# Performance work log

Hardware: AMD Instinct MI355X
Metric: run time of the kernel (lower is better)

Reference implementation:

```python
import jax, jax.numpy as jnp
import numpy as np

NUM_HEADS = 8
DIM_HEAD = 32


def setup_inputs() -> dict:
    key = jax.random.key(0)
    k1, k2, k3 = jax.random.split(key, 3)
    dim = 256
    inner = NUM_HEADS * DIM_HEAD  # 256
    x = jax.random.normal(k1, (2, dim, 32, 32, 32), dtype=jnp.float32)
    # Conv1d(kernel_size=1, bias=False) weights == plain matrices [out_ch, in_ch]
    w_qkv = jax.random.normal(k2, (inner * 3, dim), dtype=jnp.float32) * 0.02
    w_out = jax.random.normal(k3, (dim, inner), dtype=jnp.float32) * 0.02
    return {"x": x, "w_qkv": w_qkv, "w_out": w_out}


def reference(x, w_qkv, w_out):
    b, c, h, w, d = x.shape
    n = h * w * d
    x_flat = x.reshape(b, c, n)
    # 1x1 conv == channel matmul: [b, 3*inner, n]
    qkv = jnp.einsum('oc,bcn->bon', w_qkv, x_flat)
    q, k, v = jnp.split(qkv, 3, axis=1)

    def to_heads(t):  # [b, inner, n] -> [b, H, n, Dh]
        return t.reshape(b, NUM_HEADS, DIM_HEAD, n).transpose(0, 1, 3, 2)

    q = jax.nn.softmax(to_heads(q), axis=-1)   # softmax over dim_head
    k = jax.nn.softmax(to_heads(k), axis=-2)   # softmax over tokens n
    v = to_heads(v)
    # context: [b, H, Dh, Dh]
    context = jnp.einsum('bhnd,bhne->bhde', k, v)
    attn_out = jnp.einsum('bhnd,bhde->bhne', q, context)  # [b, H, n, Dh]
    attn_out = attn_out.transpose(0, 1, 3, 2).reshape(b, NUM_HEADS * DIM_HEAD, n)
    out = jnp.einsum('oi,bin->bon', w_out, attn_out)  # to_out 1x1 conv (dropout=0)
    return out.reshape(b, c, h, w, d)
```

## Files before the change

kernel.cpp:

```cpp
#include <hip/hip_runtime.h>

#define NTOK 32768

typedef __attribute__((ext_vector_type(8))) short  bf16x8;
typedef __attribute__((ext_vector_type(8))) unsigned short u16x8;
typedef __attribute__((ext_vector_type(4))) float  f32x4;

__device__ __forceinline__ unsigned short f32_to_bf16(float f) {
    unsigned int u = __float_as_uint(f);
    u += 0x7FFFu + ((u >> 16) & 1u);
    return (unsigned short)(u >> 16);
}
__device__ __forceinline__ float bf16_to_f32(unsigned short h) {
    return __uint_as_float(((unsigned int)h) << 16);
}

template <typename BT, typename CT, int MCHUNKS, bool QSOFT>
__global__ __launch_bounds__(256) void gemm_bstat(
    const unsigned short* __restrict__ A, const BT* __restrict__ B,
    CT* __restrict__ C, long sA, long sB, long sC)
{
    const int bz = blockIdx.y;
    A += (long)bz * sA; B += (long)bz * sB; C += (long)bz * sC;
    const int col0 = blockIdx.x * 64;

    __shared__ unsigned short Bs[64 * 256];

    const int t = threadIdx.x;
    const int wave = t >> 6, lane = t & 63;
    const int wm = wave >> 1, wn = wave & 1;
    const int m16 = lane & 15, quad = lane >> 4;

    {
        const int n = t & 63;
        const int kg0 = (t >> 6) * 8;
        const int key = n & 7;
        const BT* bcol = B + col0 + n;
        #pragma unroll
        for (int g = 0; g < 8; ++g) {
            const int kg = kg0 + g;
            unsigned short tmp[8];
            #pragma unroll
            for (int i = 0; i < 8; ++i) {
                BT v = bcol[(size_t)(kg * 8 + i) * NTOK];
                if constexpr (sizeof(BT) == 4) tmp[i] = f32_to_bf16((float)v);
                else                           tmp[i] = (unsigned short)v;
            }
            *(u16x8*)&Bs[n * 256 + ((kg ^ key) * 8)] = *(const u16x8*)tmp;
        }
    }
    __syncthreads();

    const int swk = m16 & 7;

    for (int mc = 0; mc < MCHUNKS; ++mc) {
        const int m0 = mc * 128;
        f32x4 acc[4][2] = {};

        const unsigned short* Abase = A + (size_t)(m0 + wm * 64 + m16) * 256 + quad * 8;

        #pragma unroll
        for (int kk = 0; kk < 8; ++kk) {
            bf16x8 bf[2];
            #pragma unroll
            for (int nt = 0; nt < 2; ++nt) {
                const int col = wn * 32 + nt * 16 + m16;
                bf[nt] = *(const bf16x8*)&Bs[col * 256 + (((kk * 4 + quad) ^ swk) * 8)];
            }
            #pragma unroll
            for (int mt = 0; mt < 4; ++mt) {
                const bf16x8 af = *(const bf16x8*)&Abase[(size_t)mt * 16 * 256 + kk * 32];
                #pragma unroll
                for (int nt = 0; nt < 2; ++nt)
                    acc[mt][nt] = __builtin_amdgcn_mfma_f32_16x16x32_bf16(
                        bf[nt], af, acc[mt][nt], 0, 0, 0);
            }
        }

        if (QSOFT && m0 < 256) {
            #pragma unroll
            for (int hj = 0; hj < 2; ++hj) {
                #pragma unroll
                for (int nt = 0; nt < 2; ++nt) {
                    #pragma unroll
                    for (int r = 0; r < 4; ++r) {
                        float mx = fmaxf(acc[hj * 2][nt][r], acc[hj * 2 + 1][nt][r]);
                        mx = fmaxf(mx, __shfl_xor(mx, 1, 64));
                        mx = fmaxf(mx, __shfl_xor(mx, 2, 64));
                        mx = fmaxf(mx, __shfl_xor(mx, 4, 64));
                        mx = fmaxf(mx, __shfl_xor(mx, 8, 64));
                        const float e0 = __expf(acc[hj * 2][nt][r] - mx);
                        const float e1 = __expf(acc[hj * 2 + 1][nt][r] - mx);
                        float s = e0 + e1;
                        s += __shfl_xor(s, 1, 64);
                        s += __shfl_xor(s, 2, 64);
                        s += __shfl_xor(s, 4, 64);
                        s += __shfl_xor(s, 8, 64);
                        const float inv = 1.0f / s;
                        acc[hj * 2][nt][r]     = e0 * inv;
                        acc[hj * 2 + 1][nt][r] = e1 * inv;
                    }
                }
            }
        }

        #pragma unroll
        for (int mt = 0; mt < 4; ++mt) {
            const int row = m0 + wm * 64 + mt * 16 + m16;
            #pragma unroll
            for (int nt = 0; nt < 2; ++nt) {
                const int col = col0 + wn * 32 + nt * 16 + quad * 4;
                if constexpr (sizeof(CT) == 4) {
                    *(float4*)&C[(size_t)row * NTOK + col] =
                        *(const float4*)&acc[mt][nt];
                } else {
                    ushort4 o;
                    o.x = f32_to_bf16(acc[mt][nt][0]);
                    o.y = f32_to_bf16(acc[mt][nt][1]);
                    o.z = f32_to_bf16(acc[mt][nt][2]);
                    o.w = f32_to_bf16(acc[mt][nt][3]);
                    *(ushort4*)&C[(size_t)row * NTOK + col] = o;
                }
            }
        }
    }
}

__global__ __launch_bounds__(256) void cast_bf16_kernel(
    const float* __restrict__ src, unsigned short* __restrict__ dst, int n4)
{
    const int i = blockIdx.x * 256 + threadIdx.x;
    if (i < n4) {
        float4 v = ((const float4*)src)[i];
        ushort4 o;
        o.x = f32_to_bf16(v.x); o.y = f32_to_bf16(v.y);
        o.z = f32_to_bf16(v.z); o.w = f32_to_bf16(v.w);
        ((ushort4*)dst)[i] = o;
    }
}

#define CCHUNK 256
__global__ __launch_bounds__(512) void ctx_mfma_kernel(
    const unsigned short* __restrict__ qkv,
    float* __restrict__ num, float* __restrict__ den)
{
    const int b = blockIdx.y;
    const int n0 = blockIdx.x * CCHUNK;
    const int h = threadIdx.x >> 6;
    const int lane = threadIdx.x & 63;
    const int m16 = lane & 15, quad = lane >> 4;

    const unsigned short* kb =
        qkv + ((long)b * 768 + 256 + h * 32 + m16) * (long)NTOK + n0 + quad * 8;
    const unsigned short* vb =
        qkv + ((long)b * 768 + 512 + h * 32 + m16) * (long)NTOK + n0 + quad * 8;

    f32x4 acc[2][2] = {};
    float dp[2] = {0.f, 0.f};

    #pragma unroll
    for (int n = 0; n < CCHUNK; n += 32) {
        bf16x8 af[2], bfv[2];
        #pragma unroll
        for (int dt = 0; dt < 2; ++dt) {
            const u16x8 kr = *(const u16x8*)(kb + (size_t)dt * 16 * NTOK + n);
            unsigned short tmp[8];
            #pragma unroll
            for (int i = 0; i < 8; ++i) {
                const float e = __expf(bf16_to_f32(kr[i]));
                const unsigned short eb = f32_to_bf16(e);
                tmp[i] = eb;
                dp[dt] += bf16_to_f32(eb);
            }
            af[dt] = *(const bf16x8*)tmp;
        }
        #pragma unroll
        for (int et = 0; et < 2; ++et)
            bfv[et] = *(const bf16x8*)(vb + (size_t)et * 16 * NTOK + n);
        #pragma unroll
        for (int dt = 0; dt < 2; ++dt)
            #pragma unroll
            for (int et = 0; et < 2; ++et)
                acc[dt][et] = __builtin_amdgcn_mfma_f32_16x16x32_bf16(
                    af[dt], bfv[et], acc[dt][et], 0, 0, 0);
    }

    float* nbase = num + ((long)(b * 8 + h) * 32) * 32;
    #pragma unroll
    for (int dt = 0; dt < 2; ++dt)
        #pragma unroll
        for (int et = 0; et < 2; ++et)
            #pragma unroll
            for (int r = 0; r < 4; ++r)
                atomicAdd(&nbase[(dt * 16 + quad * 4 + r) * 32 + et * 16 + m16],
                          acc[dt][et][r]);

    #pragma unroll
    for (int dt = 0; dt < 2; ++dt) {
        float s = dp[dt];
        s += __shfl_xor(s, 16, 64);
        s += __shfl_xor(s, 32, 64);
        if (quad == 0)
            atomicAdd(&den[b * 256 + h * 32 + dt * 16 + m16], s);
    }
}

__global__ __launch_bounds__(256) void combine_kernel(
    const float* __restrict__ w_out, const float* __restrict__ num,
    const float* __restrict__ den, unsigned short* __restrict__ W2)
{
    const int tid = blockIdx.x * 256 + threadIdx.x;
    const int b = tid >> 16;
    const int rem = tid & 65535;
    const int o = rem >> 8;
    const int i = rem & 255;
    const int h = i >> 5, d = i & 31;
    const float* wrow = w_out + o * 256 + h * 32;
    const float* nrow = num + (((long)(b * 8 + h) * 32 + d) << 5);
    float s = 0.f;
    #pragma unroll
    for (int e = 0; e < 32; ++e) s += wrow[e] * nrow[e];
    W2[tid] = f32_to_bf16(s / den[b * 256 + h * 32 + d]);
}

extern "C" void kernel_launch(void* const* d_in, const int* in_sizes, int n_in,
                              void* d_out, int out_size, void* d_ws, size_t ws_size,
                              hipStream_t stream)
{
    const float* x     = (const float*)d_in[0];
    const float* w_qkv = (const float*)d_in[1];
    const float* w_out = (const float*)d_in[2];
    float* out = (float*)d_out;

    unsigned short* qkv_bf = (unsigned short*)d_ws;
    const long qkv_elems = 2L * 768 * NTOK;
    unsigned short* wqkv_bf = qkv_bf + qkv_elems;
    unsigned short* W2 = wqkv_bf + 768 * 256;
    float* num  = (float*)(W2 + 2 * 256 * 256);
    float* den  = num + 16384;

    hipMemsetAsync(num, 0, (16384 + 512) * sizeof(float), stream);

    cast_bf16_kernel<<<192, 256, 0, stream>>>(w_qkv, wqkv_bf, 768 * 256 / 4);

    gemm_bstat<float, unsigned short, 6, true><<<dim3(512, 2), 256, 0, stream>>>(
        wqkv_bf, x, qkv_bf, 0L, 256L * NTOK, 768L * NTOK);

    ctx_mfma_kernel<<<dim3(NTOK / CCHUNK, 2), 512, 0, stream>>>(qkv_bf, num, den);

    combine_kernel<<<512, 256, 0, stream>>>(w_out, num, den, W2);

    gemm_bstat<unsigned short, float, 2, false><<<dim3(512, 2), 256, 0, stream>>>(
        W2, qkv_bf, out, 65536L, 768L * NTOK, 256L * NTOK);
}
```

Measured before the change: 287.4 us.

## Fuse QKV projection with context accumulation, keep K/V in LDS

The QKV GEMM and the K·V context reduction are merged into one kernel. K (after exp) and V tiles stay in shared memory and feed per-strip MFMA context products, so K/V are never written to or re-read from global memory. Q is stored in a strip-major layout so the output GEMM reads its strip contiguously. A-fragment loads are also software-prefetched one k-step ahead. The costs are more LDS per block (about 96KB, which lowers occupancy), many more atomicAdds on num/den (one set per 64-token strip instead of per 256), and extra register pressure.

```diff
diff --git a/kernel.cpp b/kernel.cpp
--- a/kernel.cpp
+++ b/kernel.cpp
@@ -1,6 +1,8 @@
 #include <hip/hip_runtime.h>
 
 #define NTOK 32768
+#define SSTRIP 64
+#define QSTRIDE (256 * SSTRIP)
 
 typedef __attribute__((ext_vector_type(8))) short  bf16x8;
 typedef __attribute__((ext_vector_type(8))) unsigned short u16x8;
@@ -15,16 +17,21 @@
     return __uint_as_float(((unsigned int)h) << 16);
 }
 
-template <typename BT, typename CT, int MCHUNKS, bool QSOFT>
-__global__ __launch_bounds__(256) void gemm_bstat(
-    const unsigned short* __restrict__ A, const BT* __restrict__ B,
-    CT* __restrict__ C, long sA, long sB, long sC)
+__global__ __launch_bounds__(256) void qkv_ctx_kernel(
+    const unsigned short* __restrict__ A,
+    const float* __restrict__ X,
+    unsigned short* __restrict__ Q,
+    float* __restrict__ num, float* __restrict__ den)
 {
     const int bz = blockIdx.y;
-    A += (long)bz * sA; B += (long)bz * sB; C += (long)bz * sC;
-    const int col0 = blockIdx.x * 64;
-
-    __shared__ unsigned short Bs[64 * 256];
+    X += (long)bz * 256 * NTOK;
+    Q += (long)bz * 256 * NTOK;
+    const int strip = blockIdx.x;
+    const int col0 = strip * SSTRIP;
+
+    __shared__ unsigned short Bs[SSTRIP * 256];
+    __shared__ unsigned short Ks[256 * SSTRIP];
+    __shared__ unsigned short Vs[256 * SSTRIP];
 
     const int t = threadIdx.x;
     const int wave = t >> 6, lane = t & 63;
@@ -35,17 +42,14 @@
         const int n = t & 63;
         const int kg0 = (t >> 6) * 8;
         const int key = n & 7;
-        const BT* bcol = B + col0 + n;
+        const float* bcol = X + col0 + n;
         #pragma unroll
         for (int g = 0; g < 8; ++g) {
             const int kg = kg0 + g;
             unsigned short tmp[8];
             #pragma unroll
-            for (int i = 0; i < 8; ++i) {
-                BT v = bcol[(size_t)(kg * 8 + i) * NTOK];
-                if constexpr (sizeof(BT) == 4) tmp[i] = f32_to_bf16((float)v);
-                else                           tmp[i] = (unsigned short)v;
-            }
+            for (int i = 0; i < 8; ++i)
+                tmp[i] = f32_to_bf16(bcol[(size_t)(kg * 8 + i) * NTOK]);
             *(u16x8*)&Bs[n * 256 + ((kg ^ key) * 8)] = *(const u16x8*)tmp;
         }
     }
@@ -53,14 +57,25 @@
 
     const int swk = m16 & 7;
 
-    for (int mc = 0; mc < MCHUNKS; ++mc) {
+    for (int mc = 0; mc < 6; ++mc) {
         const int m0 = mc * 128;
         f32x4 acc[4][2] = {};
 
         const unsigned short* Abase = A + (size_t)(m0 + wm * 64 + m16) * 256 + quad * 8;
 
+        bf16x8 af_cur[4], af_nxt[4];
+        #pragma unroll
+        for (int mt = 0; mt < 4; ++mt)
+            af_cur[mt] = *(const bf16x8*)&Abase[(size_t)mt * 16 * 256];
+
         #pragma unroll
         for (int kk = 0; kk < 8; ++kk) {
+            if (kk < 7) {
+                #pragma unroll
+                for (int mt = 0; mt < 4; ++mt)
+                    af_nxt[mt] = *(const bf16x8*)
+                        &Abase[(size_t)mt * 16 * 256 + (kk + 1) * 32];
+            }
             bf16x8 bf[2];
             #pragma unroll
             for (int nt = 0; nt < 2; ++nt) {
@@ -68,16 +83,16 @@
                 bf[nt] = *(const bf16x8*)&Bs[col * 256 + (((kk * 4 + quad) ^ swk) * 8)];
             }
             #pragma unroll
-            for (int mt = 0; mt < 4; ++mt) {
-                const bf16x8 af = *(const bf16x8*)&Abase[(size_t)mt * 16 * 256 + kk * 32];
+            for (int mt = 0; mt < 4; ++mt)
                 #pragma unroll
                 for (int nt = 0; nt < 2; ++nt)
                     acc[mt][nt] = __builtin_amdgcn_mfma_f32_16x16x32_bf16(
-                        bf[nt], af, acc[mt][nt], 0, 0, 0);
-            }
-        }
-
-        if (QSOFT && m0 < 256) {
+                        bf[nt], af_cur[mt], acc[mt][nt], 0, 0, 0);
+            #pragma unroll
+            for (int mt = 0; mt < 4; ++mt) af_cur[mt] = af_nxt[mt];
+        }
+
+        if (mc < 2) {
             #pragma unroll
             for (int hj = 0; hj < 2; ++hj) {
                 #pragma unroll
@@ -102,25 +117,177 @@
                     }
                 }
             }
-        }
-
-        #pragma unroll
-        for (int mt = 0; mt < 4; ++mt) {
-            const int row = m0 + wm * 64 + mt * 16 + m16;
-            #pragma unroll
-            for (int nt = 0; nt < 2; ++nt) {
-                const int col = col0 + wn * 32 + nt * 16 + quad * 4;
-                if constexpr (sizeof(CT) == 4) {
-                    *(float4*)&C[(size_t)row * NTOK + col] =
-                        *(const float4*)&acc[mt][nt];
-                } else {
+            unsigned short* Qb = Q + (size_t)strip * QSTRIDE;
+            #pragma unroll
+            for (int mt = 0; mt < 4; ++mt) {
+                const int row = m0 + wm * 64 + mt * 16 + m16;
+                #pragma unroll
+                for (int nt = 0; nt < 2; ++nt) {
+                    const int col = wn * 32 + nt * 16 + quad * 4;
                     ushort4 o;
                     o.x = f32_to_bf16(acc[mt][nt][0]);
                     o.y = f32_to_bf16(acc[mt][nt][1]);
                     o.z = f32_to_bf16(acc[mt][nt][2]);
                     o.w = f32_to_bf16(acc[mt][nt][3]);
-                    *(ushort4*)&C[(size_t)row * NTOK + col] = o;
+                    *(ushort4*)&Qb[(size_t)row * SSTRIP + col] = o;
                 }
+            }
+        } else if (mc < 4) {
+            #pragma unroll
+            for (int mt = 0; mt < 4; ++mt) {
+                const int kchan = (m0 - 256) + wm * 64 + mt * 16 + m16;
+                float dp = 0.f;
+                #pragma unroll
+                for (int nt = 0; nt < 2; ++nt) {
+                    ushort4 o;
+                    unsigned short eb;
+                    #pragma unroll
+                    for (int r = 0; r < 4; ++r) {
+                        eb = f32_to_bf16(__expf(acc[mt][nt][r]));
+                        dp += bf16_to_f32(eb);
+                        ((unsigned short*)&o)[r] = eb;
+                    }
+                    const int col = wn * 32 + nt * 16 + quad * 4;
+                    *(ushort4*)&Ks[(size_t)kchan * SSTRIP + col] = o;
+                }
+                dp += __shfl_xor(dp, 16, 64);
+                dp += __shfl_xor(dp, 32, 64);
+                if (quad == 0)
+                    atomicAdd(&den[bz * 256 + kchan], dp);
+            }
+        } else {
+            #pragma unroll
+            for (int mt = 0; mt < 4; ++mt) {
+                const int vchan = (m0 - 512) + wm * 64 + mt * 16 + m16;
+                #pragma unroll
+                for (int nt = 0; nt < 2; ++nt) {
+                    ushort4 o;
+                    o.x = f32_to_bf16(acc[mt][nt][0]);
+                    o.y = f32_to_bf16(acc[mt][nt][1]);
+                    o.z = f32_to_bf16(acc[mt][nt][2]);
+                    o.w = f32_to_bf16(acc[mt][nt][3]);
+                    const int col = wn * 32 + nt * 16 + quad * 4;
+                    *(ushort4*)&Vs[(size_t)vchan * SSTRIP + col] = o;
+                }
+            }
+        }
+    }
+
+    __syncthreads();
+
+    #pragma unroll
+    for (int hh = 0; hh < 2; ++hh) {
+        const int h = wave * 2 + hh;
+        f32x4 cacc[2][2] = {};
+        #pragma unroll
+        for (int ks = 0; ks < 2; ++ks) {
+            bf16x8 kf[2], vf[2];
+            #pragma unroll
+            for (int dt = 0; dt < 2; ++dt)
+                kf[dt] = *(const bf16x8*)
+                    &Ks[(size_t)(h * 32 + dt * 16 + m16) * SSTRIP + ks * 32 + quad * 8];
+            #pragma unroll
+            for (int et = 0; et < 2; ++et)
+                vf[et] = *(const bf16x8*)
+                    &Vs[(size_t)(h * 32 + et * 16 + m16) * SSTRIP + ks * 32 + quad * 8];
+            #pragma unroll
+            for (int dt = 0; dt < 2; ++dt)
+                #pragma unroll
+                for (int et = 0; et < 2; ++et)
+                    cacc[dt][et] = __builtin_amdgcn_mfma_f32_16x16x32_bf16(
+                        kf[dt], vf[et], cacc[dt][et], 0, 0, 0);
+        }
+        float* nbase = num + ((long)(bz * 8 + h) * 32) * 32;
+        #pragma unroll
+        for (int dt = 0; dt < 2; ++dt)
+            #pragma unroll
+            for (int et = 0; et < 2; ++et)
+                #pragma unroll
+                for (int r = 0; r < 4; ++r)
+                    atomicAdd(&nbase[(dt * 16 + quad * 4 + r) * 32 + et * 16 + m16],
+                              cacc[dt][et][r]);
+    }
+}
+
+__global__ __launch_bounds__(256) void gemm_out(
+    const unsigned short* __restrict__ A,
+    const unsigned short* __restrict__ Q,
+    float* __restrict__ C)
+{
+    const int bz = blockIdx.y;
+    A += (long)bz * 65536;
+    Q += (long)bz * 256 * NTOK;
+    C += (long)bz * 256 * NTOK;
+    const int strip = blockIdx.x;
+    const int col0 = strip * SSTRIP;
+
+    __shared__ unsigned short Bs[SSTRIP * 256];
+
+    const int t = threadIdx.x;
+    const int wave = t >> 6, lane = t & 63;
+    const int wm = wave >> 1, wn = wave & 1;
+    const int m16 = lane & 15, quad = lane >> 4;
+
+    {
+        const int n = t & 63;
+        const int kg0 = (t >> 6) * 8;
+        const int key = n & 7;
+        const unsigned short* bcol = Q + (size_t)strip * QSTRIDE + n;
+        #pragma unroll
+        for (int g = 0; g < 8; ++g) {
+            const int kg = kg0 + g;
+            unsigned short tmp[8];
+            #pragma unroll
+            for (int i = 0; i < 8; ++i)
+                tmp[i] = bcol[(size_t)(kg * 8 + i) * SSTRIP];
+            *(u16x8*)&Bs[n * 256 + ((kg ^ key) * 8)] = *(const u16x8*)tmp;
+        }
+    }
+    __syncthreads();
+
+    const int swk = m16 & 7;
+
+    for (int mc = 0; mc < 2; ++mc) {
+        const int m0 = mc * 128;
+        f32x4 acc[4][2] = {};
+        const unsigned short* Abase = A + (size_t)(m0 + wm * 64 + m16) * 256 + quad * 8;
+
+        bf16x8 af_cur[4], af_nxt[4];
+        #pragma unroll
+        for (int mt = 0; mt < 4; ++mt)
+            af_cur[mt] = *(const bf16x8*)&Abase[(size_t)mt * 16 * 256];
+
+        #pragma unroll
+        for (int kk = 0; kk < 8; ++kk) {
+            if (kk < 7) {
+                #pragma unroll
+                for (int mt = 0; mt < 4; ++mt)
+                    af_nxt[mt] = *(const bf16x8*)
+                        &Abase[(size_t)mt * 16 * 256 + (kk + 1) * 32];
+            }
+            bf16x8 bf[2];
+            #pragma unroll
+            for (int nt = 0; nt < 2; ++nt) {
+                const int col = wn * 32 + nt * 16 + m16;
+                bf[nt] = *(const bf16x8*)&Bs[col * 256 + (((kk * 4 + quad) ^ swk) * 8)];
+            }
+            #pragma unroll
+            for (int mt = 0; mt < 4; ++mt)
+                #pragma unroll
+                for (int nt = 0; nt < 2; ++nt)
+                    acc[mt][nt] = __builtin_amdgcn_mfma_f32_16x16x32_bf16(
+                        bf[nt], af_cur[mt], acc[mt][nt], 0, 0, 0);
+            #pragma unroll
+            for (int mt = 0; mt < 4; ++mt) af_cur[mt] = af_nxt[mt];
+        }
+
+        #pragma unroll
+        for (int mt = 0; mt < 4; ++mt) {
+            const int row = m0 + wm * 64 + mt * 16 + m16;
+            #pragma unroll
+            for (int nt = 0; nt < 2; ++nt) {
+                const int col = col0 + wn * 32 + nt * 16 + quad * 4;
+                *(float4*)&C[(size_t)row * NTOK + col] = *(const float4*)&acc[mt][nt];
             }
         }
     }
@@ -136,72 +303,6 @@
         o.x = f32_to_bf16(v.x); o.y = f32_to_bf16(v.y);
         o.z = f32_to_bf16(v.z); o.w = f32_to_bf16(v.w);
         ((ushort4*)dst)[i] = o;
-    }
-}
-
-#define CCHUNK 256
-__global__ __launch_bounds__(512) void ctx_mfma_kernel(
-    const unsigned short* __restrict__ qkv,
-    float* __restrict__ num, float* __restrict__ den)
-{
-    const int b = blockIdx.y;
-    const int n0 = blockIdx.x * CCHUNK;
-    const int h = threadIdx.x >> 6;
-    const int lane = threadIdx.x & 63;
-    const int m16 = lane & 15, quad = lane >> 4;
-
-    const unsigned short* kb =
-        qkv + ((long)b * 768 + 256 + h * 32 + m16) * (long)NTOK + n0 + quad * 8;
-    const unsigned short* vb =
-        qkv + ((long)b * 768 + 512 + h * 32 + m16) * (long)NTOK + n0 + quad * 8;
-
-    f32x4 acc[2][2] = {};
-    float dp[2] = {0.f, 0.f};
-
-    #pragma unroll
-    for (int n = 0; n < CCHUNK; n += 32) {
-        bf16x8 af[2], bfv[2];
-        #pragma unroll
-        for (int dt = 0; dt < 2; ++dt) {
-            const u16x8 kr = *(const u16x8*)(kb + (size_t)dt * 16 * NTOK + n);
-            unsigned short tmp[8];
-            #pragma unroll
-            for (int i = 0; i < 8; ++i) {
-                const float e = __expf(bf16_to_f32(kr[i]));
-                const unsigned short eb = f32_to_bf16(e);
-                tmp[i] = eb;
-                dp[dt] += bf16_to_f32(eb);
-            }
-            af[dt] = *(const bf16x8*)tmp;
-        }
-        #pragma unroll
-        for (int et = 0; et < 2; ++et)
-            bfv[et] = *(const bf16x8*)(vb + (size_t)et * 16 * NTOK + n);
-        #pragma unroll
-        for (int dt = 0; dt < 2; ++dt)
-            #pragma unroll
-            for (int et = 0; et < 2; ++et)
-                acc[dt][et] = __builtin_amdgcn_mfma_f32_16x16x32_bf16(
-                    af[dt], bfv[et], acc[dt][et], 0, 0, 0);
-    }
-
-    float* nbase = num + ((long)(b * 8 + h) * 32) * 32;
-    #pragma unroll
-    for (int dt = 0; dt < 2; ++dt)
-        #pragma unroll
-        for (int et = 0; et < 2; ++et)
-            #pragma unroll
-            for (int r = 0; r < 4; ++r)
-                atomicAdd(&nbase[(dt * 16 + quad * 4 + r) * 32 + et * 16 + m16],
-                          acc[dt][et][r]);
-
-    #pragma unroll
-    for (int dt = 0; dt < 2; ++dt) {
-        float s = dp[dt];
-        s += __shfl_xor(s, 16, 64);
-        s += __shfl_xor(s, 32, 64);
-        if (quad == 0)
-            atomicAdd(&den[b * 256 + h * 32 + dt * 16 + m16], s);
     }
 }
 
@@ -232,9 +333,8 @@
     const float* w_out = (const float*)d_in[2];
     float* out = (float*)d_out;
 
-    unsigned short* qkv_bf = (unsigned short*)d_ws;
-    const long qkv_elems = 2L * 768 * NTOK;
-    unsigned short* wqkv_bf = qkv_bf + qkv_elems;
+    unsigned short* q_bf = (unsigned short*)d_ws;
+    unsigned short* wqkv_bf = q_bf + 2L * 256 * NTOK;
     unsigned short* W2 = wqkv_bf + 768 * 256;
     float* num  = (float*)(W2 + 2 * 256 * 256);
     float* den  = num + 16384;
@@ -243,13 +343,10 @@
 
     cast_bf16_kernel<<<192, 256, 0, stream>>>(w_qkv, wqkv_bf, 768 * 256 / 4);
 
-    gemm_bstat<float, unsigned short, 6, true><<<dim3(512, 2), 256, 0, stream>>>(
-        wqkv_bf, x, qkv_bf, 0L, 256L * NTOK, 768L * NTOK);
-
-    ctx_mfma_kernel<<<dim3(NTOK / CCHUNK, 2), 512, 0, stream>>>(qkv_bf, num, den);
+    qkv_ctx_kernel<<<dim3(NTOK / SSTRIP, 2), 256, 0, stream>>>(
+        wqkv_bf, x, q_bf, num, den);
 
     combine_kernel<<<512, 256, 0, stream>>>(w_out, num, den, W2);
 
-    gemm_bstat<unsigned short, float, 2, false><<<dim3(512, 2), 256, 0, stream>>>(
-        W2, qkv_bf, out, 65536L, 768L * NTOK, 256L * NTOK);
-}
+    gemm_out<<<dim3(NTOK / SSTRIP, 2), 256, 0, stream>>>(W2, q_bf, out);
+}
```

New measurement: 301.4 us. 4.9% more time.
